# Performance work log

Hardware: AMD Instinct MI355X
Metric: run time of the kernel (lower is better)

The kernel has to match this reference:

```python
import jax, jax.numpy as jnp
import numpy as np

VOCAB = 50000
B, T, D_OUT = 32, 512, 256
E_DIMS = (300, 300, 200)


def setup_inputs() -> dict:
    key = jax.random.key(0)
    ks = jax.random.split(key, 8)
    ids = jax.random.randint(ks[0], (B, T), 0, VOCAB)
    E0 = jax.random.normal(ks[1], (VOCAB, E_DIMS[0]), dtype=jnp.float32)
    E1 = jax.random.normal(ks[2], (VOCAB, E_DIMS[1]), dtype=jnp.float32)
    E2 = jax.random.normal(ks[3], (VOCAB, E_DIMS[2]), dtype=jnp.float32)
    # Glorot-ish scaled projection weights
    W0 = jax.random.normal(ks[4], (E_DIMS[0], D_OUT), dtype=jnp.float32) / np.sqrt(E_DIMS[0])
    W1 = jax.random.normal(ks[5], (E_DIMS[1], D_OUT), dtype=jnp.float32) / np.sqrt(E_DIMS[1])
    W2 = jax.random.normal(ks[6], (E_DIMS[2], D_OUT), dtype=jnp.float32) / np.sqrt(E_DIMS[2])
    Wa = jax.random.normal(ks[7], (D_OUT, 1), dtype=jnp.float32) / np.sqrt(D_OUT)
    return {
        "ids": ids,
        "E0": E0, "E1": E1, "E2": E2,
        "W0": W0, "b0": jnp.zeros((D_OUT,), jnp.float32),
        "W1": W1, "b1": jnp.zeros((D_OUT,), jnp.float32),
        "W2": W2, "b2": jnp.zeros((D_OUT,), jnp.float32),
        "Wa": Wa, "ba": jnp.zeros((1,), jnp.float32),
    }


def reference(ids, E0, E1, E2, W0, b0, W1, b1, W2, b2, Wa, ba):
    # Per-source embedding gather + Dense projection -> [B, T, D_OUT]
    p0 = E0[ids] @ W0 + b0
    p1 = E1[ids] @ W1 + b1
    p2 = E2[ids] @ W2 + b2
    projected = jnp.stack([p0, p1, p2], axis=2)  # [B, T, n_emb, D]
    # Attention Dense(1) over D, softmax over the n_emb axis
    logits = jnp.einsum('btnd,do->btno', projected, Wa) + ba  # [B, T, n, 1]
    alphas = jax.nn.softmax(logits, axis=2)
    # Weighted combine: matmul(projected^T, alphas) then squeeze -> [B, T, D]
    out = jnp.einsum('btnd,btn->btd', projected, alphas[..., 0])
    return out
```

## Files before the change

### kernel.cpp

```cpp
#include <hip/hip_runtime.h>
#include <hip/hip_bf16.h>

typedef __attribute__((ext_vector_type(8))) short short8;
typedef __attribute__((ext_vector_type(4))) float floatx4;
typedef unsigned short ushort_t;
typedef unsigned int uint_t;

#define DOUT   256
#define KPAD   864
#define XPITCH 872
#define TB     32
#define NTOK   16384
#define NPREP_T 27
#define NPREP_U 217

static __device__ inline ushort_t f2bf(float f) {
    union { float f; uint_t u; } a; a.f = f;
    uint_t u = a.u;
    return (ushort_t)((u + 0x7FFFu + ((u >> 16) & 1u)) >> 16);
}
static __device__ inline uint_t pack2bf(float x, float y) {
    return (uint_t)f2bf(x) | ((uint_t)f2bf(y) << 16);
}

__global__ __launch_bounds__(256) void k_prep(
    const float* __restrict__ W0, const float* __restrict__ W1,
    const float* __restrict__ W2,
    const float* __restrict__ b0, const float* __restrict__ b1,
    const float* __restrict__ b2,
    const float* __restrict__ Wa, const float* __restrict__ ba,
    float* __restrict__ u, float* __restrict__ lb, ushort_t* __restrict__ Wt)
{
    __shared__ ushort_t tile[32][256];
    int tid = threadIdx.x;
    if (blockIdx.x < NPREP_T) {
        int k0 = blockIdx.x * 32;
        for (int idx = tid; idx < 32 * 256; idx += 256) {
            int kk = idx >> 8, d = idx & 255;
            int kp = k0 + kk;
            float v = 0.f;
            const float* src = nullptr;
            if (kp < 320)      { if (kp < 300) src = W0 + kp * DOUT; }
            else if (kp < 640) { int o = kp - 320; if (o < 300) src = W1 + o * DOUT; }
            else               { int o = kp - 640; if (o < 200) src = W2 + o * DOUT; }
            if (src) v = src[d];
            tile[kk][d] = f2bf(v);
        }
        __syncthreads();
        int d = tid;
        #pragma unroll
        for (int g = 0; g < 4; ++g) {
            union { uint4 v; ushort_t s[8]; } p;
            #pragma unroll
            for (int j = 0; j < 8; ++j) p.s[j] = tile[g * 8 + j][d];
            *(uint4*)(Wt + (size_t)d * KPAD + k0 + g * 8) = p.v;
        }
    } else {
        int lane = tid & 63;
        int w = tid >> 6;
        int kp = (blockIdx.x - NPREP_T) * 4 + w;
        if (kp > 866) return;
        const float* row = nullptr;
        if (kp < 320)       { if (kp < 300) row = W0 + kp * DOUT; }
        else if (kp < 640)  { int o = kp - 320; if (o < 300) row = W1 + o * DOUT; }
        else if (kp < 864)  { int o = kp - 640; if (o < 200) row = W2 + o * DOUT; }
        else                { int n = kp - 864; row = (n == 0) ? b0 : ((n == 1) ? b1 : b2); }
        float acc = 0.f;
        if (row) {
            #pragma unroll
            for (int j = lane; j < DOUT; j += 64)
                acc += row[j] * Wa[j];
        }
        for (int off = 32; off > 0; off >>= 1) acc += __shfl_down(acc, off);
        if (lane == 0) {
            if (kp < 864) u[kp] = acc;
            else          lb[kp - 864] = acc + ba[0];
        }
    }
}

#define MFMA_STEP(ACC, KC) {                                                   \
    short8 a0 = *(const short8*)&Xs[mrow][(KC) + kg8];                         \
    short8 a1 = *(const short8*)&Xs[16 + mrow][(KC) + kg8];                    \
    short8 bv0 = *(const short8*)(bp0 + (KC));                                 \
    short8 bv1 = *(const short8*)(bp1 + (KC));                                 \
    ACC[0][0] = __builtin_amdgcn_mfma_f32_16x16x32_bf16(a0, bv0, ACC[0][0], 0, 0, 0); \
    ACC[1][0] = __builtin_amdgcn_mfma_f32_16x16x32_bf16(a1, bv0, ACC[1][0], 0, 0, 0); \
    ACC[0][1] = __builtin_amdgcn_mfma_f32_16x16x32_bf16(a0, bv1, ACC[0][1], 0, 0, 0); \
    ACC[1][1] = __builtin_amdgcn_mfma_f32_16x16x32_bf16(a1, bv1, ACC[1][1], 0, 0, 0); \
}

__global__ __launch_bounds__(512, 4) void k_main(
    const int* __restrict__ ids,
    const float* __restrict__ E0, const float* __restrict__ E1,
    const float* __restrict__ E2,
    const float* __restrict__ b0, const float* __restrict__ b1,
    const float* __restrict__ b2,
    const float* __restrict__ u, const float* __restrict__ lb,
    const ushort_t* __restrict__ Wt,
    float* __restrict__ out)
{
    __shared__ __align__(16) ushort_t Xs[TB][XPITCH];
    __shared__ float alphaS[TB][4];

    int tid = threadIdx.x;
    int tok0 = blockIdx.x * TB;

    int trow = tid >> 4, sub = tid & 15;
    int id = ids[tok0 + trow];
    uint2* Xd2 = (uint2*)&Xs[trow][0];
    const float4* E0v = (const float4*)E0;
    const float4* E1v = (const float4*)E1;
    const float4* E2v = (const float4*)E2;
    float l0 = 0.f, l1 = 0.f, l2 = 0.f;

    #pragma unroll
    for (int i = sub; i < 75; i += 16) {
        float4 t = E0v[(size_t)id * 75 + i];
        float4 uu = *(const float4*)(u + 4 * i);
        l0 += t.x * uu.x + t.y * uu.y + t.z * uu.z + t.w * uu.w;
        Xd2[i] = make_uint2(pack2bf(t.x, t.y), pack2bf(t.z, t.w));
    }
    #pragma unroll
    for (int i = sub; i < 75; i += 16) {
        float4 t = E1v[(size_t)id * 75 + i];
        float4 uu = *(const float4*)(u + 320 + 4 * i);
        l1 += t.x * uu.x + t.y * uu.y + t.z * uu.z + t.w * uu.w;
        Xd2[80 + i] = make_uint2(pack2bf(t.x, t.y), pack2bf(t.z, t.w));
    }
    #pragma unroll
    for (int i = sub; i < 50; i += 16) {
        float4 t = E2v[(size_t)id * 50 + i];
        float4 uu = *(const float4*)(u + 640 + 4 * i);
        l2 += t.x * uu.x + t.y * uu.y + t.z * uu.z + t.w * uu.w;
        Xd2[160 + i] = make_uint2(pack2bf(t.x, t.y), pack2bf(t.z, t.w));
    }
    uint2 z2 = make_uint2(0u, 0u);
    for (int i = 75 + sub;  i < 80;  i += 16) Xd2[i] = z2;
    for (int i = 155 + sub; i < 160; i += 16) Xd2[i] = z2;
    for (int i = 210 + sub; i < 218; i += 16) Xd2[i] = z2;

    #pragma unroll
    for (int off = 8; off > 0; off >>= 1) {
        l0 += __shfl_down(l0, off);
        l1 += __shfl_down(l1, off);
        l2 += __shfl_down(l2, off);
    }
    if (sub == 0) {
        l0 += lb[0]; l1 += lb[1]; l2 += lb[2];
        float m = fmaxf(l0, fmaxf(l1, l2));
        float e0 = __expf(l0 - m), e1 = __expf(l1 - m), e2 = __expf(l2 - m);
        float inv = 1.f / (e0 + e1 + e2);
        alphaS[trow][0] = e0 * inv;
        alphaS[trow][1] = e1 * inv;
        alphaS[trow][2] = e2 * inv;
    }
    __syncthreads();

    int lane = tid & 63;
    int w = tid >> 6;
    int mrow = lane & 15;
    int kg8 = (lane >> 4) * 8;

    const ushort_t* bp0 = Wt + (size_t)(w * 32 +  0 + mrow) * KPAD + kg8;
    const ushort_t* bp1 = Wt + (size_t)(w * 32 + 16 + mrow) * KPAD + kg8;

    floatx4 acc0[2][2], acc1[2][2], acc2[2][2];
    #pragma unroll
    for (int mt = 0; mt < 2; ++mt)
        #pragma unroll
        for (int nt = 0; nt < 2; ++nt) {
            floatx4 z = {0.f, 0.f, 0.f, 0.f};
            acc0[mt][nt] = z; acc1[mt][nt] = z; acc2[mt][nt] = z;
        }

    #pragma unroll
    for (int kc = 0; kc < 320; kc += 32)   MFMA_STEP(acc0, kc);
    #pragma unroll
    for (int kc = 320; kc < 640; kc += 32) MFMA_STEP(acc1, kc);
    #pragma unroll
    for (int kc = 640; kc < 864; kc += 32) MFMA_STEP(acc2, kc);

    float bb0[2], bb1[2], bb2[2];
    #pragma unroll
    for (int nt = 0; nt < 2; ++nt) {
        int n = w * 32 + nt * 16 + mrow;
        bb0[nt] = b0[n];
        bb1[nt] = b1[n];
        bb2[nt] = b2[n];
    }
    #pragma unroll
    for (int mt = 0; mt < 2; ++mt) {
        #pragma unroll
        for (int r = 0; r < 4; ++r) {
            int tok = mt * 16 + (lane >> 4) * 4 + r;
            float a0 = alphaS[tok][0], a1 = alphaS[tok][1], a2 = alphaS[tok][2];
            size_t rowoff = (size_t)(tok0 + tok) * DOUT;
            #pragma unroll
            for (int nt = 0; nt < 2; ++nt) {
                int n = w * 32 + nt * 16 + mrow;
                float v = a0 * (acc0[mt][nt][r] + bb0[nt])
                        + a1 * (acc1[mt][nt][r] + bb1[nt])
                        + a2 * (acc2[mt][nt][r] + bb2[nt]);
                out[rowoff + n] = v;
            }
        }
    }
}

extern "C" void kernel_launch(void* const* d_in, const int* in_sizes, int n_in,
                              void* d_out, int out_size, void* d_ws, size_t ws_size,
                              hipStream_t stream) {
    const int*   ids = (const int*)d_in[0];
    const float* E0  = (const float*)d_in[1];
    const float* E1  = (const float*)d_in[2];
    const float* E2  = (const float*)d_in[3];
    const float* W0  = (const float*)d_in[4];
    const float* b0  = (const float*)d_in[5];
    const float* W1  = (const float*)d_in[6];
    const float* b1  = (const float*)d_in[7];
    const float* W2  = (const float*)d_in[8];
    const float* b2  = (const float*)d_in[9];
    const float* Wa  = (const float*)d_in[10];
    const float* ba  = (const float*)d_in[11];

    float* u     = (float*)d_ws;
    float* lb    = u + KPAD;
    ushort_t* Wt = (ushort_t*)((char*)d_ws + 4096);

    k_prep<<<NPREP_T + NPREP_U, 256, 0, stream>>>(W0, W1, W2, b0, b1, b2, Wa, ba,
                                                  u, lb, Wt);
    k_main<<<NTOK / TB, 512, 0, stream>>>(ids, E0, E1, E2, b0, b1, b2, u, lb, Wt,
                                          (float*)d_out);
}
```

Baseline: 205.2 us.

## Halve token tile, widen per-wave N tile, batch embedding gathers into registers

The main kernel now processes 16 tokens per block with 256 threads, and each wave computes 64 output columns with a single A fragment reused across four B fragments. All embedding-row loads are issued up front into a register array before the packing and logit work, which raises memory-level parallelism for the gather. The u vector is padded so that zero-filled tails are read rather than explicitly written, and bf16 conversion uses the HIP intrinsic. Smaller blocks double the number of W reads from L2 per token and the register footprint grows, but more blocks can be resident.

```diff
diff --git a/kernel.cpp b/kernel.cpp
--- a/kernel.cpp
+++ b/kernel.cpp
@@ -8,19 +8,15 @@
 
 #define DOUT   256
 #define KPAD   864
-#define XPITCH 872
-#define TB     32
+#define XPITCH 904
+#define TB     16
 #define NTOK   16384
 #define NPREP_T 27
-#define NPREP_U 217
-
-static __device__ inline ushort_t f2bf(float f) {
-    union { float f; uint_t u; } a; a.f = f;
-    uint_t u = a.u;
-    return (ushort_t)((u + 0x7FFFu + ((u >> 16) & 1u)) >> 16);
-}
+#define NPREP_U 225
+
 static __device__ inline uint_t pack2bf(float x, float y) {
-    return (uint_t)f2bf(x) | ((uint_t)f2bf(y) << 16);
+    __hip_bfloat162 h = __float22bfloat162_rn(make_float2(x, y));
+    return *(uint_t*)&h;
 }
 
 __global__ __launch_bounds__(256) void k_prep(
@@ -44,7 +40,7 @@
             else if (kp < 640) { int o = kp - 320; if (o < 300) src = W1 + o * DOUT; }
             else               { int o = kp - 640; if (o < 200) src = W2 + o * DOUT; }
             if (src) v = src[d];
-            tile[kk][d] = f2bf(v);
+            tile[kk][d] = (ushort_t)(pack2bf(v, 0.f) & 0xFFFFu);
         }
         __syncthreads();
         int d = tid;
@@ -59,12 +55,12 @@
         int lane = tid & 63;
         int w = tid >> 6;
         int kp = (blockIdx.x - NPREP_T) * 4 + w;
-        if (kp > 866) return;
+        if (kp > 898) return;
         const float* row = nullptr;
         if (kp < 320)       { if (kp < 300) row = W0 + kp * DOUT; }
         else if (kp < 640)  { int o = kp - 320; if (o < 300) row = W1 + o * DOUT; }
         else if (kp < 864)  { int o = kp - 640; if (o < 200) row = W2 + o * DOUT; }
-        else                { int n = kp - 864; row = (n == 0) ? b0 : ((n == 1) ? b1 : b2); }
+        else if (kp >= 896) { int n = kp - 896; row = (n == 0) ? b0 : ((n == 1) ? b1 : b2); }
         float acc = 0.f;
         if (row) {
             #pragma unroll
@@ -73,24 +69,22 @@
         }
         for (int off = 32; off > 0; off >>= 1) acc += __shfl_down(acc, off);
         if (lane == 0) {
-            if (kp < 864) u[kp] = acc;
-            else          lb[kp - 864] = acc + ba[0];
+            if (kp < 896) u[kp] = acc;
+            else          lb[kp - 896] = acc + ba[0];
         }
     }
 }
 
 #define MFMA_STEP(ACC, KC) {                                                   \
     short8 a0 = *(const short8*)&Xs[mrow][(KC) + kg8];                         \
-    short8 a1 = *(const short8*)&Xs[16 + mrow][(KC) + kg8];                    \
-    short8 bv0 = *(const short8*)(bp0 + (KC));                                 \
-    short8 bv1 = *(const short8*)(bp1 + (KC));                                 \
-    ACC[0][0] = __builtin_amdgcn_mfma_f32_16x16x32_bf16(a0, bv0, ACC[0][0], 0, 0, 0); \
-    ACC[1][0] = __builtin_amdgcn_mfma_f32_16x16x32_bf16(a1, bv0, ACC[1][0], 0, 0, 0); \
-    ACC[0][1] = __builtin_amdgcn_mfma_f32_16x16x32_bf16(a0, bv1, ACC[0][1], 0, 0, 0); \
-    ACC[1][1] = __builtin_amdgcn_mfma_f32_16x16x32_bf16(a1, bv1, ACC[1][1], 0, 0, 0); \
-}
-
-__global__ __launch_bounds__(512, 4) void k_main(
+    _Pragma("unroll")                                                          \
+    for (int nt = 0; nt < 4; ++nt) {                                           \
+        short8 bv = *(const short8*)(bp[nt] + (KC));                           \
+        ACC[nt] = __builtin_amdgcn_mfma_f32_16x16x32_bf16(a0, bv, ACC[nt], 0, 0, 0); \
+    }                                                                          \
+}
+
+__global__ __launch_bounds__(256, 5) void k_main(
     const int* __restrict__ ids,
     const float* __restrict__ E0, const float* __restrict__ E1,
     const float* __restrict__ E2,
@@ -112,33 +106,49 @@
     const float4* E0v = (const float4*)E0;
     const float4* E1v = (const float4*)E1;
     const float4* E2v = (const float4*)E2;
+    float4 f4z = make_float4(0.f, 0.f, 0.f, 0.f);
+
+    float4 g[14];
+    {
+        const float4* p0 = E0v + (size_t)id * 75;
+        const float4* p1 = E1v + (size_t)id * 75;
+        const float4* p2 = E2v + (size_t)id * 50;
+        g[0] = p0[sub];      g[1] = p0[sub + 16];
+        g[2] = p0[sub + 32]; g[3] = p0[sub + 48];
+        g[4] = (sub < 11) ? p0[sub + 64] : f4z;
+        g[5] = p1[sub];      g[6] = p1[sub + 16];
+        g[7] = p1[sub + 32]; g[8] = p1[sub + 48];
+        g[9] = (sub < 11) ? p1[sub + 64] : f4z;
+        g[10] = p2[sub];      g[11] = p2[sub + 16];
+        g[12] = p2[sub + 32];
+        g[13] = (sub < 2) ? p2[sub + 48] : f4z;
+    }
+
     float l0 = 0.f, l1 = 0.f, l2 = 0.f;
-
-    #pragma unroll
-    for (int i = sub; i < 75; i += 16) {
-        float4 t = E0v[(size_t)id * 75 + i];
+    #pragma unroll
+    for (int j = 0; j < 5; ++j) {
+        int i = sub + 16 * j;
+        float4 t = g[j];
         float4 uu = *(const float4*)(u + 4 * i);
         l0 += t.x * uu.x + t.y * uu.y + t.z * uu.z + t.w * uu.w;
         Xd2[i] = make_uint2(pack2bf(t.x, t.y), pack2bf(t.z, t.w));
     }
     #pragma unroll
-    for (int i = sub; i < 75; i += 16) {
-        float4 t = E1v[(size_t)id * 75 + i];
+    for (int j = 0; j < 5; ++j) {
+        int i = sub + 16 * j;
+        float4 t = g[5 + j];
         float4 uu = *(const float4*)(u + 320 + 4 * i);
         l1 += t.x * uu.x + t.y * uu.y + t.z * uu.z + t.w * uu.w;
         Xd2[80 + i] = make_uint2(pack2bf(t.x, t.y), pack2bf(t.z, t.w));
     }
     #pragma unroll
-    for (int i = sub; i < 50; i += 16) {
-        float4 t = E2v[(size_t)id * 50 + i];
+    for (int j = 0; j < 4; ++j) {
+        int i = sub + 16 * j;
+        float4 t = g[10 + j];
         float4 uu = *(const float4*)(u + 640 + 4 * i);
         l2 += t.x * uu.x + t.y * uu.y + t.z * uu.z + t.w * uu.w;
         Xd2[160 + i] = make_uint2(pack2bf(t.x, t.y), pack2bf(t.z, t.w));
     }
-    uint2 z2 = make_uint2(0u, 0u);
-    for (int i = 75 + sub;  i < 80;  i += 16) Xd2[i] = z2;
-    for (int i = 155 + sub; i < 160; i += 16) Xd2[i] = z2;
-    for (int i = 210 + sub; i < 218; i += 16) Xd2[i] = z2;
 
     #pragma unroll
     for (int off = 8; off > 0; off >>= 1) {
@@ -162,17 +172,17 @@
     int mrow = lane & 15;
     int kg8 = (lane >> 4) * 8;
 
-    const ushort_t* bp0 = Wt + (size_t)(w * 32 +  0 + mrow) * KPAD + kg8;
-    const ushort_t* bp1 = Wt + (size_t)(w * 32 + 16 + mrow) * KPAD + kg8;
-
-    floatx4 acc0[2][2], acc1[2][2], acc2[2][2];
-    #pragma unroll
-    for (int mt = 0; mt < 2; ++mt)
-        #pragma unroll
-        for (int nt = 0; nt < 2; ++nt) {
-            floatx4 z = {0.f, 0.f, 0.f, 0.f};
-            acc0[mt][nt] = z; acc1[mt][nt] = z; acc2[mt][nt] = z;
-        }
+    const ushort_t* bp[4];
+    #pragma unroll
+    for (int nt = 0; nt < 4; ++nt)
+        bp[nt] = Wt + (size_t)(w * 64 + nt * 16 + mrow) * KPAD + kg8;
+
+    floatx4 acc0[4], acc1[4], acc2[4];
+    #pragma unroll
+    for (int nt = 0; nt < 4; ++nt) {
+        floatx4 z = {0.f, 0.f, 0.f, 0.f};
+        acc0[nt] = z; acc1[nt] = z; acc2[nt] = z;
+    }
 
     #pragma unroll
     for (int kc = 0; kc < 320; kc += 32)   MFMA_STEP(acc0, kc);
@@ -181,29 +191,26 @@
     #pragma unroll
     for (int kc = 640; kc < 864; kc += 32) MFMA_STEP(acc2, kc);
 
-    float bb0[2], bb1[2], bb2[2];
-    #pragma unroll
-    for (int nt = 0; nt < 2; ++nt) {
-        int n = w * 32 + nt * 16 + mrow;
+    float bb0[4], bb1[4], bb2[4];
+    #pragma unroll
+    for (int nt = 0; nt < 4; ++nt) {
+        int n = w * 64 + nt * 16 + mrow;
         bb0[nt] = b0[n];
         bb1[nt] = b1[n];
         bb2[nt] = b2[n];
     }
     #pragma unroll
-    for (int mt = 0; mt < 2; ++mt) {
+    for (int r = 0; r < 4; ++r) {
+        int tok = (lane >> 4) * 4 + r;
+        float a0 = alphaS[tok][0], a1 = alphaS[tok][1], a2 = alphaS[tok][2];
+        size_t rowoff = (size_t)(tok0 + tok) * DOUT;
         #pragma unroll
-        for (int r = 0; r < 4; ++r) {
-            int tok = mt * 16 + (lane >> 4) * 4 + r;
-            float a0 = alphaS[tok][0], a1 = alphaS[tok][1], a2 = alphaS[tok][2];
-            size_t rowoff = (size_t)(tok0 + tok) * DOUT;
-            #pragma unroll
-            for (int nt = 0; nt < 2; ++nt) {
-                int n = w * 32 + nt * 16 + mrow;
-                float v = a0 * (acc0[mt][nt][r] + bb0[nt])
-                        + a1 * (acc1[mt][nt][r] + bb1[nt])
-                        + a2 * (acc2[mt][nt][r] + bb2[nt]);
-                out[rowoff + n] = v;
-            }
+        for (int nt = 0; nt < 4; ++nt) {
+            int n = w * 64 + nt * 16 + mrow;
+            float v = a0 * (acc0[nt][r] + bb0[nt])
+                    + a1 * (acc1[nt][r] + bb1[nt])
+                    + a2 * (acc2[nt][r] + bb2[nt]);
+            out[rowoff + n] = v;
         }
     }
 }
@@ -225,11 +232,11 @@
     const float* ba  = (const float*)d_in[11];
 
     float* u     = (float*)d_ws;
-    float* lb    = u + KPAD;
+    float* lb    = u + 896;
     ushort_t* Wt = (ushort_t*)((char*)d_ws + 4096);
 
     k_prep<<<NPREP_T + NPREP_U, 256, 0, stream>>>(W0, W1, W2, b0, b1, b2, Wa, ba,
                                                   u, lb, Wt);
-    k_main<<<NTOK / TB, 512, 0, stream>>>(ids, E0, E1, E2, b0, b1, b2, u, lb, Wt,
+    k_main<<<NTOK / TB, 256, 0, stream>>>(ids, E0, E1, E2, b0, b1, b2, u, lb, Wt,
                                           (float*)d_out);
 }
```

New measurement: 213.3 us. 3.9% more time.
